# Performance work log

Measured on AMD Instinct MI355X. Metric: run time of the kernel, lower is better.

The kernel has to match this reference:

```python
import jax, jax.numpy as jnp
import numpy as np

MAX_NUM_LEVELS = 3.5
NUM_LEVELS = 4  # mip levels 0..3 (levels clamped to [0, 2.5])


def affine_grid(matrix, N, H, W):
    # F.affine_grid, align_corners=False. matrix: (N,2,3) -> grid (N,H,W,2) in xy order.
    xs = (jnp.arange(W, dtype=jnp.float32) + 0.5) * (2.0 / W) - 1.0
    ys = (jnp.arange(H, dtype=jnp.float32) + 0.5) * (2.0 / H) - 1.0
    gy, gx = jnp.meshgrid(ys, xs, indexing='ij')
    base = jnp.stack([gx, gy, jnp.ones_like(gx)], axis=-1)  # (H,W,3)
    return jnp.einsum('hwk,nik->nhwi', base, matrix)  # (N,H,W,2)


def grid_sample_border(img, grid):
    # bilinear grid_sample, padding_mode='border', align_corners=False
    N, C, H, W = img.shape
    x = (grid[..., 0] + 1.0) * (W / 2.0) - 0.5
    y = (grid[..., 1] + 1.0) * (H / 2.0) - 0.5
    x0 = jnp.floor(x); y0 = jnp.floor(y)
    tx = x - x0; ty = y - y0
    x0i = jnp.clip(x0.astype(jnp.int32), 0, W - 1)
    x1i = jnp.clip(x0.astype(jnp.int32) + 1, 0, W - 1)
    y0i = jnp.clip(y0.astype(jnp.int32), 0, H - 1)
    y1i = jnp.clip(y0.astype(jnp.int32) + 1, 0, H - 1)
    b = jnp.arange(N)[:, None, None]
    g = lambda yi, xi: img[b, :, yi, xi]  # (N,Ho,Wo,C) gather
    out = (g(y0i, x0i) * ((1 - tx) * (1 - ty))[..., None]
           + g(y0i, x1i) * (tx * (1 - ty))[..., None]
           + g(y1i, x0i) * ((1 - tx) * ty)[..., None]
           + g(y1i, x1i) * (tx * ty)[..., None])
    return jnp.transpose(out, (0, 3, 1, 2))  # (N,C,Ho,Wo)


def blur_downsample(x):
    N, C, H, W = x.shape
    k1 = jnp.array([1., 3., 3., 1.], dtype=x.dtype) / 8.0
    k = k1[:, None] * k1[None, :]
    xp = jnp.pad(x, ((0, 0), (0, 0), (1, 2), (1, 2)), mode='reflect')
    kernel = jnp.broadcast_to(k[None, None], (C, 1, 4, 4))
    return jax.lax.conv_general_dilated(xp, kernel, window_strides=(2, 2), padding='VALID',
                                        feature_group_count=C,
                                        dimension_numbers=('NCHW', 'OIHW', 'NCHW'))


def compute_levels(grid, H, W):
    # per-pixel mip LOD from local stretch of the sampling grid (in source pixel units)
    coords = (grid + 1.0) * 0.5 * jnp.array([W, H], dtype=grid.dtype)  # (N,Ho,Wo,2)
    dx = coords[:, :-1, 1:] - coords[:, :-1, :-1]
    dy = coords[:, 1:, :-1] - coords[:, :-1, :-1]
    scale = jnp.maximum(jnp.linalg.norm(dx, axis=-1), jnp.linalg.norm(dy, axis=-1))
    scale = jnp.pad(scale, ((0, 0), (0, 1), (0, 1)), mode='edge')  # (N,Ho,Wo)
    levels = jnp.log2(jnp.maximum(scale, 1.0))
    return jnp.clip(levels, 0.0, MAX_NUM_LEVELS - 1.0)


def mipmap_warp(img, grid):
    N, C, H, W = img.shape
    levels = compute_levels(grid, H, W)  # (N,Ho,Wo)
    pyr = [img]
    for _ in range(NUM_LEVELS - 1):
        pyr.append(blur_downsample(pyr[-1]))
    samples = jnp.stack([grid_sample_border(p, grid) for p in pyr], axis=0)  # (L,N,C,Ho,Wo)
    ls = jnp.arange(NUM_LEVELS, dtype=levels.dtype)[:, None, None, None]
    w = jnp.clip(1.0 - jnp.abs(levels[None] - ls), 0.0, 1.0)  # trilinear blend weights (L,N,Ho,Wo)
    return jnp.einsum('lnhw,lnchw->nchw', w, samples)


def setup_inputs() -> dict:
    key = jax.random.key(0)
    k1, k2, k3 = jax.random.split(key, 3)
    N, C, H, W, D = 64, 3, 256, 256, 512
    img = jax.random.normal(k1, (N, C, H, W), dtype=jnp.float32)
    features = jax.random.normal(k2, (N, D), dtype=jnp.float32)
    # learned head params (zero-init in torch; small random here so the warp is nontrivial)
    lin_w = jax.random.normal(k3, (4, D), dtype=jnp.float32) * 0.02
    lin_b = jnp.zeros((4,), dtype=jnp.float32)
    return {'img': img, 'features': features, 'lin_w': lin_w, 'lin_b': lin_b}


def reference(img, features, lin_w, lin_b):
    params = features @ lin_w.T + lin_b  # (N,4)
    rot = jnp.tanh(params[:, 0:1]) * jnp.pi
    scale = jnp.exp(params[:, 1:2])
    sx, sy = params[:, 2:3], params[:, 3:4]
    c, s = jnp.cos(rot), jnp.sin(rot)
    matrix = jnp.concatenate([scale * c, -scale * s, sx, scale * s, scale * c, sy], axis=1).reshape(-1, 2, 3)
    affine_params = jnp.concatenate([rot, scale, sx, sy], axis=1)
    N, C, H, W = img.shape
    grid = affine_grid(matrix, N, H, W)
    out = mipmap_warp(img, grid)
    return out, grid, matrix, affine_params
```

## Files before the change

### kernel.cpp

```cpp
#include <hip/hip_runtime.h>
#include <math.h>

#define N_B 64
#define C_CH 3
#define H_IMG 256
#define W_IMG 256
#define D_FEAT 512

#define OUT_OFF_GRID   12582912
#define OUT_OFF_MATRIX 20971520
#define OUT_OFF_AFFINE 20971904

#define PYR1_SZ (N_B * 128 * 128 * 3)
#define PYR2_SZ (N_B * 64 * 64 * 3)
#define PYR3_SZ (N_B * 32 * 32 * 3)

typedef float v2f __attribute__((ext_vector_type(2)));
typedef float f4u __attribute__((ext_vector_type(4), aligned(4)));
typedef float f2u __attribute__((ext_vector_type(2), aligned(4)));

__global__ void params_kernel(const float* __restrict__ features,
                              const float* __restrict__ lin_w,
                              const float* __restrict__ lin_b,
                              float* __restrict__ out_matrix,
                              float* __restrict__ out_affine,
                              float* __restrict__ ws_params)
{
    const int n = blockIdx.x;
    const int t = threadIdx.x;
    const float* f = features + n * D_FEAT;
    float f0 = f[t];
    float f1 = f[t + 256];
    float a0 = f0 * lin_w[0 * D_FEAT + t] + f1 * lin_w[0 * D_FEAT + t + 256];
    float a1 = f0 * lin_w[1 * D_FEAT + t] + f1 * lin_w[1 * D_FEAT + t + 256];
    float a2 = f0 * lin_w[2 * D_FEAT + t] + f1 * lin_w[2 * D_FEAT + t + 256];
    float a3 = f0 * lin_w[3 * D_FEAT + t] + f1 * lin_w[3 * D_FEAT + t + 256];

    __shared__ float red[4][256];
    red[0][t] = a0; red[1][t] = a1; red[2][t] = a2; red[3][t] = a3;
    __syncthreads();
    for (int s = 128; s > 0; s >>= 1) {
        if (t < s) {
            red[0][t] += red[0][t + s];
            red[1][t] += red[1][t + s];
            red[2][t] += red[2][t + s];
            red[3][t] += red[3][t + s];
        }
        __syncthreads();
    }
    if (t == 0) {
        float p0 = red[0][0] + lin_b[0];
        float p1 = red[1][0] + lin_b[1];
        float p2 = red[2][0] + lin_b[2];
        float p3 = red[3][0] + lin_b[3];
        float rot   = tanhf(p0) * 3.14159265358979323846f;
        float scale = expf(p1);
        float c = cosf(rot), s = sinf(rot);
        float m00 = scale * c, m01 = -scale * s, m02 = p2;
        float m10 = scale * s, m11 =  scale * c, m12 = p3;
        out_matrix[n * 6 + 0] = m00;
        out_matrix[n * 6 + 1] = m01;
        out_matrix[n * 6 + 2] = m02;
        out_matrix[n * 6 + 3] = m10;
        out_matrix[n * 6 + 4] = m11;
        out_matrix[n * 6 + 5] = m12;
        out_affine[n * 4 + 0] = rot;
        out_affine[n * 4 + 1] = scale;
        out_affine[n * 4 + 2] = p2;
        out_affine[n * 4 + 3] = p3;
        float lv = log2f(fmaxf(scale, 1.0f));
        lv = fminf(fmaxf(lv, 0.0f), 2.5f);
        ws_params[n * 8 + 0] = m00;
        ws_params[n * 8 + 1] = m01;
        ws_params[n * 8 + 2] = m02;
        ws_params[n * 8 + 3] = m10;
        ws_params[n * 8 + 4] = m11;
        ws_params[n * 8 + 5] = m12;
        ws_params[n * 8 + 6] = lv;
        ws_params[n * 8 + 7] = 0.0f;
    }
}

__global__ void down1_kernel(const float* __restrict__ img,
                             float* __restrict__ pyr1,
                             const float* __restrict__ ws_params)
{
    const int n = blockIdx.y;
    if (ws_params[n * 8 + 6] <= 0.0f) return;
    const int p = blockIdx.x * 256 + threadIdx.x;
    const int i = p >> 7;
    const int j = p & 127;

    int r[4];
#pragma unroll
    for (int a = 0; a < 4; a++) {
        int q = 2 * i + a - 1;
        if (q < 0) q = -q;
        if (q >= 256) q = 510 - q;
        r[a] = q;
    }
    const int  cb  = min(max(2 * j - 1, 0), 252);
    const bool jlo = (j == 0);
    const bool jhi = (j == 127);
    const bool je  = jlo || jhi;

    const float* s = img + (size_t)n * 3 * 65536;

    f4u T[3][4];
#pragma unroll
    for (int c = 0; c < 3; c++)
#pragma unroll
        for (int a = 0; a < 4; a++)
            T[c][a] = *(const f4u*)(s + c * 65536 + r[a] * 256 + cb);

    const float k0 = 0.125f, k1 = 0.375f;
    const float kr[4] = {0.125f, 0.375f, 0.375f, 0.125f};
    float o[3];
#pragma unroll
    for (int c = 0; c < 3; c++) {
        float acc = 0.0f;
#pragma unroll
        for (int a = 0; a < 4; a++) {
            f4u A = T[c][a];
            float t0 = je  ? A.y : A.x;
            float t1 = jlo ? A.x : (jhi ? A.z : A.y);
            float t2 = jlo ? A.y : (jhi ? A.w : A.z);
            float t3 = je  ? A.z : A.w;
            float h = k0 * t0 + k1 * t1 + k1 * t2 + k0 * t3;
            acc += kr[a] * h;
        }
        o[c] = acc;
    }
    float* d = pyr1 + (size_t)n * (128 * 128 * 3) + (size_t)p * 3;
    d[0] = o[0]; d[1] = o[1]; d[2] = o[2];
}

template<int Hs, int Ws>
__global__ void downN_kernel(const float* __restrict__ src,
                             float* __restrict__ dst,
                             const float* __restrict__ ws_params,
                             float lvl_gate)
{
    const int n = blockIdx.y;
    if (ws_params[n * 8 + 6] <= lvl_gate) return;
    constexpr int Hd = Hs / 2, Wd = Ws / 2;
    const int p = blockIdx.x * 256 + threadIdx.x;
    const int i = p / Wd;
    const int j = p % Wd;

    int r[4], cc[4];
#pragma unroll
    for (int a = 0; a < 4; a++) {
        int q = 2 * i + a - 1;
        if (q < 0) q = -q;
        if (q >= Hs) q = 2 * Hs - 2 - q;
        r[a] = q;
        int u = 2 * j + a - 1;
        if (u < 0) u = -u;
        if (u >= Ws) u = 2 * Ws - 2 - u;
        cc[a] = u;
    }
    const float* s = src + (size_t)n * 3 * Hs * Ws;
    const int rs = 3 * Ws;

    f4u T[4][4];
#pragma unroll
    for (int a = 0; a < 4; a++)
#pragma unroll
        for (int b = 0; b < 4; b++)
            T[a][b] = *(const f4u*)(s + r[a] * rs + 3 * cc[b]);

    const float k0 = 0.125f, k1 = 0.375f;
    const float kr[4] = {0.125f, 0.375f, 0.375f, 0.125f};
    float o[3];
#pragma unroll
    for (int c = 0; c < 3; c++) {
        float acc = 0.0f;
#pragma unroll
        for (int a = 0; a < 4; a++) {
            float h = k0 * T[a][0][c] + k1 * T[a][1][c]
                    + k1 * T[a][2][c] + k0 * T[a][3][c];
            acc += kr[a] * h;
        }
        o[c] = acc;
    }
    float* d = dst + (size_t)n * 3 * Hd * Wd + (size_t)p * 3;
    d[0] = o[0]; d[1] = o[1]; d[2] = o[2];
}

struct TapSetup {
    const float* row0;
    const float* row1;
    float w00, w01, w10, w11;
    bool selHi0, selLo1;
    size_t planeStride;
};

__device__ __forceinline__ TapSetup make_taps(const float* __restrict__ base, int l,
                                              float X, float Y)
{
    const int Wl = W_IMG >> l;
    const int Hl = H_IMG >> l;
    float x = (X + 1.0f) * (0.5f * (float)Wl) - 0.5f;
    float y = (Y + 1.0f) * (0.5f * (float)Hl) - 0.5f;
    float x0f = floorf(x), y0f = floorf(y);
    float tx = x - x0f, ty = y - y0f;
    int x0 = (int)x0f, y0 = (int)y0f;
    int y0i = min(max(y0,     0), Hl - 1);
    int y1i = min(max(y0 + 1, 0), Hl - 1);
    int xp = min(max(x0, 0), Wl - 2);
    TapSetup ts;
    ts.row0 = base + (size_t)y0i * Wl + xp;
    ts.row1 = base + (size_t)y1i * Wl + xp;
    ts.selHi0 = (x0 >= Wl - 1);
    ts.selLo1 = (x0 < 0);
    ts.w00 = (1.0f - tx) * (1.0f - ty);
    ts.w01 = tx * (1.0f - ty);
    ts.w10 = (1.0f - tx) * ty;
    ts.w11 = tx * ty;
    ts.planeStride = (size_t)Hl * Wl;
    return ts;
}

__device__ __forceinline__ float tap_eval(const TapSetup& ts, float2 a, float2 b)
{
    float t00 = ts.selHi0 ? a.y : a.x;
    float t01 = ts.selLo1 ? a.x : a.y;
    float t10 = ts.selHi0 ? b.y : b.x;
    float t11 = ts.selLo1 ? b.x : b.y;
    return ts.w00 * t00 + ts.w01 * t01 + ts.w10 * t10 + ts.w11 * t11;
}

struct NTap {
    const float* r0;
    const float* r1;
    float w00, w01, w10, w11;
    bool hi, lo;
};

__device__ __forceinline__ NTap make_ntap(const float* __restrict__ base, int l,
                                          float X, float Y)
{
    const int Wl = W_IMG >> l;
    const int Hl = H_IMG >> l;
    float x = (X + 1.0f) * (0.5f * (float)Wl) - 0.5f;
    float y = (Y + 1.0f) * (0.5f * (float)Hl) - 0.5f;
    float x0f = floorf(x), y0f = floorf(y);
    float tx = x - x0f, ty = y - y0f;
    int x0 = (int)x0f, y0 = (int)y0f;
    int y0i = min(max(y0,     0), Hl - 1);
    int y1i = min(max(y0 + 1, 0), Hl - 1);
    int xp  = min(max(x0, 0), Wl - 2);
    const int rs = 3 * Wl;
    NTap t;
    t.r0 = base + (size_t)y0i * rs + 3 * xp;
    t.r1 = base + (size_t)y1i * rs + 3 * xp;
    t.hi = (x0 >= Wl - 1);
    t.lo = (x0 < 0);
    t.w00 = (1.0f - tx) * (1.0f - ty);
    t.w01 = tx * (1.0f - ty);
    t.w10 = (1.0f - tx) * ty;
    t.w11 = tx * ty;
    return t;
}

__device__ __forceinline__ void ntap_eval(const NTap& t, f4u a, f2u a2,
                                          f4u b, f2u b2, float* v)
{
    float e0[6] = {a.x, a.y, a.z, a.w, a2.x, a2.y};
    float e1[6] = {b.x, b.y, b.z, b.w, b2.x, b2.y};
#pragma unroll
    for (int c = 0; c < 3; c++) {
        float p00 = t.hi ? e0[c + 3] : e0[c];
        float p01 = t.lo ? e0[c]     : e0[c + 3];
        float p10 = t.hi ? e1[c + 3] : e1[c];
        float p11 = t.lo ? e1[c]     : e1[c + 3];
        v[c] = t.w00 * p00 + t.w01 * p01 + t.w10 * p10 + t.w11 * p11;
    }
}

__device__ __forceinline__ const float* npyr(int l, const float* p1,
                                             const float* p2, const float* p3,
                                             int n)
{
    if (l == 1) return p1 + (size_t)n * (128 * 128 * 3);
    if (l == 2) return p2 + (size_t)n * (64 * 64 * 3);
    return p3 + (size_t)n * (32 * 32 * 3);
}

__global__ __launch_bounds__(256, 4)
void warp_kernel(const float* __restrict__ img,
                 const float* __restrict__ pyr1,
                 const float* __restrict__ pyr2,
                 const float* __restrict__ pyr3,
                 const float* __restrict__ ws_params,
                 float* __restrict__ out,
                 float* __restrict__ gridOut)
{
    const int n = blockIdx.y;
    const int tile = blockIdx.x;
    const int tid = threadIdx.x;
    const int w0 = (tile & 7) << 5;
    const int h0 = (tile >> 3) << 3;
    const int w = w0 + (((tid >> 6) & 1) << 4) + (tid & 15);
    const int h = h0 + ((tid >> 7) << 2) + ((tid >> 4) & 3);

    const float* P = ws_params + n * 8;
    float m00 = P[0], m01 = P[1], m02 = P[2];
    float m10 = P[3], m11 = P[4], m12 = P[5];
    float lv  = P[6];

    float gx = ((float)w + 0.5f) * (2.0f / (float)W_IMG) - 1.0f;
    float gy = ((float)h + 0.5f) * (2.0f / (float)H_IMG) - 1.0f;
    float X = m00 * gx + m01 * gy + m02;
    float Y = m10 * gx + m11 * gy + m12;

    v2f gp = {X, Y};
    __builtin_nontemporal_store(gp, (v2f*)gridOut + ((size_t)(n * H_IMG + h) * W_IMG + w));

    int   l0   = (int)lv;
    float frac = lv - (float)l0;
    const bool hasL1 = (frac > 0.0f);
    const float wA = 1.0f - frac;

    size_t obase = ((size_t)n * C_CH * H_IMG + h) * W_IMG + w;

    if (l0 == 0) {
        const float* base0 = img + (size_t)n * 3 * 65536;
        TapSetup t0 = make_taps(base0, 0, X, Y);
        float2 A0[3], B0[3];
#pragma unroll
        for (int c = 0; c < 3; c++) {
            A0[c] = *(const float2*)(t0.row0 + c * t0.planeStride);
            B0[c] = *(const float2*)(t0.row1 + c * t0.planeStride);
        }
        if (hasL1) {
            NTap t1 = make_ntap(pyr1 + (size_t)n * (128 * 128 * 3), 1, X, Y);
            f4u a = *(const f4u*)t1.r0;  f2u a2 = *(const f2u*)(t1.r0 + 4);
            f4u b = *(const f4u*)t1.r1;  f2u b2 = *(const f2u*)(t1.r1 + 4);
            float v1[3];
            ntap_eval(t1, a, a2, b, b2, v1);
#pragma unroll
            for (int c = 0; c < 3; c++) {
                float v0 = tap_eval(t0, A0[c], B0[c]);
                __builtin_nontemporal_store(wA * v0 + frac * v1[c],
                                            out + obase + (size_t)c * 65536);
            }
        } else {
#pragma unroll
            for (int c = 0; c < 3; c++)
                __builtin_nontemporal_store(tap_eval(t0, A0[c], B0[c]),
                                            out + obase + (size_t)c * 65536);
        }
    } else {
        const float* base0 = npyr(l0, pyr1, pyr2, pyr3, n);
        NTap t0 = make_ntap(base0, l0, X, Y);
        f4u a = *(const f4u*)t0.r0;  f2u a2 = *(const f2u*)(t0.r0 + 4);
        f4u b = *(const f4u*)t0.r1;  f2u b2 = *(const f2u*)(t0.r1 + 4);
        if (hasL1) {
            const float* base1 = npyr(l0 + 1, pyr1, pyr2, pyr3, n);
            NTap t1 = make_ntap(base1, l0 + 1, X, Y);
            f4u c1 = *(const f4u*)t1.r0;  f2u c2 = *(const f2u*)(t1.r0 + 4);
            f4u d1 = *(const f4u*)t1.r1;  f2u d2 = *(const f2u*)(t1.r1 + 4);
            float v0[3], v1[3];
            ntap_eval(t0, a, a2, b, b2, v0);
            ntap_eval(t1, c1, c2, d1, d2, v1);
#pragma unroll
            for (int c = 0; c < 3; c++)
                __builtin_nontemporal_store(wA * v0[c] + frac * v1[c],
                                            out + obase + (size_t)c * 65536);
        } else {
            float v0[3];
            ntap_eval(t0, a, a2, b, b2, v0);
#pragma unroll
            for (int c = 0; c < 3; c++)
                __builtin_nontemporal_store(v0[c],
                                            out + obase + (size_t)c * 65536);
        }
    }
}

extern "C" void kernel_launch(void* const* d_in, const int* in_sizes, int n_in,
                              void* d_out, int out_size, void* d_ws, size_t ws_size,
                              hipStream_t stream)
{
    const float* img      = (const float*)d_in[0];
    const float* features = (const float*)d_in[1];
    const float* lin_w    = (const float*)d_in[2];
    const float* lin_b    = (const float*)d_in[3];

    float* out        = (float*)d_out;
    float* gridOut    = out + OUT_OFF_GRID;
    float* out_matrix = out + OUT_OFF_MATRIX;
    float* out_affine = out + OUT_OFF_AFFINE;

    float* ws        = (float*)d_ws;
    float* ws_params = ws;
    float* pyr1 = ws + 1024;
    float* pyr2 = pyr1 + PYR1_SZ;
    float* pyr3 = pyr2 + PYR2_SZ;

    params_kernel<<<N_B, 256, 0, stream>>>(features, lin_w, lin_b,
                                           out_matrix, out_affine, ws_params);

    down1_kernel<<<dim3(64, N_B), 256, 0, stream>>>(img, pyr1, ws_params);
    downN_kernel<128, 128><<<dim3(16, N_B), 256, 0, stream>>>(pyr1, pyr2, ws_params, 1.0f);
    downN_kernel<64, 64><<<dim3(4, N_B), 256, 0, stream>>>(pyr2, pyr3, ws_params, 2.0f);

    warp_kernel<<<dim3(H_IMG * W_IMG / 256, N_B), 256, 0, stream>>>(
        img, pyr1, pyr2, pyr3, ws_params, out, gridOut);
}
```

Baseline: 166.7 us.

## Compute four outputs per thread in down1 and two rows per thread in warp

The first downsample kernel now has each thread produce four adjacent level-1 pixels from two vector loads plus two edge scalars per row. This shares horizontal taps across outputs and writes results with three 16-byte stores instead of scattered scalar stores. The warp kernel processes two output rows per thread (rows h and h+8), halving the grid and issuing both sets of loads before evaluating them to raise memory-level parallelism. The cost is higher register pressure under the existing launch bounds and fewer blocks per kernel.

```diff
diff --git a/kernel.cpp b/kernel.cpp
--- a/kernel.cpp
+++ b/kernel.cpp
@@ -87,9 +87,9 @@
 {
     const int n = blockIdx.y;
     if (ws_params[n * 8 + 6] <= 0.0f) return;
-    const int p = blockIdx.x * 256 + threadIdx.x;
-    const int i = p >> 7;
-    const int j = p & 127;
+    const int idx = blockIdx.x * 256 + threadIdx.x;
+    const int t = idx & 31;
+    const int i = idx >> 5;
 
     int r[4];
 #pragma unroll
@@ -99,40 +99,48 @@
         if (q >= 256) q = 510 - q;
         r[a] = q;
     }
-    const int  cb  = min(max(2 * j - 1, 0), 252);
-    const bool jlo = (j == 0);
-    const bool jhi = (j == 127);
-    const bool je  = jlo || jhi;
+    const int c8 = 8 * t;
+    const int li = (t > 0)  ? c8 - 1 : 1;
+    const int ri = (t < 31) ? c8 + 8 : 254;
 
     const float* s = img + (size_t)n * 3 * 65536;
-
-    f4u T[3][4];
-#pragma unroll
-    for (int c = 0; c < 3; c++)
-#pragma unroll
-        for (int a = 0; a < 4; a++)
-            T[c][a] = *(const f4u*)(s + c * 65536 + r[a] * 256 + cb);
 
     const float k0 = 0.125f, k1 = 0.375f;
     const float kr[4] = {0.125f, 0.375f, 0.375f, 0.125f};
-    float o[3];
-#pragma unroll
-    for (int c = 0; c < 3; c++) {
-        float acc = 0.0f;
-#pragma unroll
-        for (int a = 0; a < 4; a++) {
-            f4u A = T[c][a];
-            float t0 = je  ? A.y : A.x;
-            float t1 = jlo ? A.x : (jhi ? A.z : A.y);
-            float t2 = jlo ? A.y : (jhi ? A.w : A.z);
-            float t3 = je  ? A.z : A.w;
-            float h = k0 * t0 + k1 * t1 + k1 * t2 + k0 * t3;
-            acc += kr[a] * h;
-        }
-        o[c] = acc;
-    }
-    float* d = pyr1 + (size_t)n * (128 * 128 * 3) + (size_t)p * 3;
-    d[0] = o[0]; d[1] = o[1]; d[2] = o[2];
+
+    float acc[3][4] = {};
+#pragma unroll
+    for (int a = 0; a < 4; a++) {
+        const float* rbase = s + (size_t)r[a] * 256;
+        f4u A[3], B[3];
+        float L[3], R[3];
+#pragma unroll
+        for (int c = 0; c < 3; c++) {
+            const float* row = rbase + c * 65536;
+            A[c] = *(const f4u*)(row + c8);
+            B[c] = *(const f4u*)(row + c8 + 4);
+            L[c] = row[li];
+            R[c] = row[ri];
+        }
+#pragma unroll
+        for (int c = 0; c < 3; c++) {
+            float h0 = k0 * L[c]   + k1 * A[c].x + k1 * A[c].y + k0 * A[c].z;
+            float h1 = k0 * A[c].y + k1 * A[c].z + k1 * A[c].w + k0 * B[c].x;
+            float h2 = k0 * A[c].w + k1 * B[c].x + k1 * B[c].y + k0 * B[c].z;
+            float h3 = k0 * B[c].y + k1 * B[c].z + k1 * B[c].w + k0 * R[c];
+            acc[c][0] += kr[a] * h0;
+            acc[c][1] += kr[a] * h1;
+            acc[c][2] += kr[a] * h2;
+            acc[c][3] += kr[a] * h3;
+        }
+    }
+    float* d = pyr1 + (size_t)n * (128 * 128 * 3) + ((size_t)i * 128 + 4 * t) * 3;
+    f4u s0 = {acc[0][0], acc[1][0], acc[2][0], acc[0][1]};
+    f4u s1 = {acc[1][1], acc[2][1], acc[0][2], acc[1][2]};
+    f4u s2 = {acc[2][2], acc[0][3], acc[1][3], acc[2][3]};
+    *(f4u*)(d)     = s0;
+    *(f4u*)(d + 4) = s1;
+    *(f4u*)(d + 8) = s2;
 }
 
 template<int Hs, int Ws>
@@ -264,11 +272,20 @@
     return t;
 }
 
-__device__ __forceinline__ void ntap_eval(const NTap& t, f4u a, f2u a2,
-                                          f4u b, f2u b2, float* v)
-{
-    float e0[6] = {a.x, a.y, a.z, a.w, a2.x, a2.y};
-    float e1[6] = {b.x, b.y, b.z, b.w, b2.x, b2.y};
+struct NPay { f4u a; f2u a2; f4u b; f2u b2; };
+
+__device__ __forceinline__ NPay ntap_load(const NTap& t)
+{
+    NPay p;
+    p.a  = *(const f4u*)t.r0;  p.a2 = *(const f2u*)(t.r0 + 4);
+    p.b  = *(const f4u*)t.r1;  p.b2 = *(const f2u*)(t.r1 + 4);
+    return p;
+}
+
+__device__ __forceinline__ void ntap_eval(const NTap& t, const NPay& p, float* v)
+{
+    float e0[6] = {p.a.x, p.a.y, p.a.z, p.a.w, p.a2.x, p.a2.y};
+    float e1[6] = {p.b.x, p.b.y, p.b.z, p.b.w, p.b2.x, p.b2.y};
 #pragma unroll
     for (int c = 0; c < 3; c++) {
         float p00 = t.hi ? e0[c + 3] : e0[c];
@@ -301,81 +318,111 @@
     const int tile = blockIdx.x;
     const int tid = threadIdx.x;
     const int w0 = (tile & 7) << 5;
-    const int h0 = (tile >> 3) << 3;
-    const int w = w0 + (((tid >> 6) & 1) << 4) + (tid & 15);
-    const int h = h0 + ((tid >> 7) << 2) + ((tid >> 4) & 3);
+    const int h0 = (tile >> 3) << 4;
+    const int w  = w0 + (((tid >> 6) & 1) << 4) + (tid & 15);
+    const int ha = h0 + ((tid >> 7) << 2) + ((tid >> 4) & 3);
+    const int hb = ha + 8;
 
     const float* P = ws_params + n * 8;
     float m00 = P[0], m01 = P[1], m02 = P[2];
     float m10 = P[3], m11 = P[4], m12 = P[5];
     float lv  = P[6];
 
-    float gx = ((float)w + 0.5f) * (2.0f / (float)W_IMG) - 1.0f;
-    float gy = ((float)h + 0.5f) * (2.0f / (float)H_IMG) - 1.0f;
-    float X = m00 * gx + m01 * gy + m02;
-    float Y = m10 * gx + m11 * gy + m12;
-
-    v2f gp = {X, Y};
-    __builtin_nontemporal_store(gp, (v2f*)gridOut + ((size_t)(n * H_IMG + h) * W_IMG + w));
+    float gx  = ((float)w + 0.5f) * (2.0f / (float)W_IMG) - 1.0f;
+    float gya = ((float)ha + 0.5f) * (2.0f / (float)H_IMG) - 1.0f;
+    float gyb = ((float)hb + 0.5f) * (2.0f / (float)H_IMG) - 1.0f;
+    float Xa = m00 * gx + m01 * gya + m02;
+    float Ya = m10 * gx + m11 * gya + m12;
+    float Xb = m00 * gx + m01 * gyb + m02;
+    float Yb = m10 * gx + m11 * gyb + m12;
+
+    v2f gpa = {Xa, Ya}, gpb = {Xb, Yb};
+    __builtin_nontemporal_store(gpa, (v2f*)gridOut + ((size_t)(n * H_IMG + ha) * W_IMG + w));
+    __builtin_nontemporal_store(gpb, (v2f*)gridOut + ((size_t)(n * H_IMG + hb) * W_IMG + w));
 
     int   l0   = (int)lv;
     float frac = lv - (float)l0;
     const bool hasL1 = (frac > 0.0f);
     const float wA = 1.0f - frac;
 
-    size_t obase = ((size_t)n * C_CH * H_IMG + h) * W_IMG + w;
+    size_t oba = ((size_t)n * C_CH * H_IMG + ha) * W_IMG + w;
+    size_t obb = ((size_t)n * C_CH * H_IMG + hb) * W_IMG + w;
 
     if (l0 == 0) {
         const float* base0 = img + (size_t)n * 3 * 65536;
-        TapSetup t0 = make_taps(base0, 0, X, Y);
-        float2 A0[3], B0[3];
+        TapSetup ta = make_taps(base0, 0, Xa, Ya);
+        TapSetup tb = make_taps(base0, 0, Xb, Yb);
+        float2 Aa[3], Ba[3], Ab[3], Bb[3];
 #pragma unroll
         for (int c = 0; c < 3; c++) {
-            A0[c] = *(const float2*)(t0.row0 + c * t0.planeStride);
-            B0[c] = *(const float2*)(t0.row1 + c * t0.planeStride);
+            Aa[c] = *(const float2*)(ta.row0 + c * 65536);
+            Ba[c] = *(const float2*)(ta.row1 + c * 65536);
+        }
+#pragma unroll
+        for (int c = 0; c < 3; c++) {
+            Ab[c] = *(const float2*)(tb.row0 + c * 65536);
+            Bb[c] = *(const float2*)(tb.row1 + c * 65536);
         }
         if (hasL1) {
-            NTap t1 = make_ntap(pyr1 + (size_t)n * (128 * 128 * 3), 1, X, Y);
-            f4u a = *(const f4u*)t1.r0;  f2u a2 = *(const f2u*)(t1.r0 + 4);
-            f4u b = *(const f4u*)t1.r1;  f2u b2 = *(const f2u*)(t1.r1 + 4);
-            float v1[3];
-            ntap_eval(t1, a, a2, b, b2, v1);
+            const float* b1 = pyr1 + (size_t)n * (128 * 128 * 3);
+            NTap ua = make_ntap(b1, 1, Xa, Ya);
+            NTap ub = make_ntap(b1, 1, Xb, Yb);
+            NPay pa = ntap_load(ua);
+            NPay pb = ntap_load(ub);
+            float v1a[3], v1b[3];
+            ntap_eval(ua, pa, v1a);
+            ntap_eval(ub, pb, v1b);
 #pragma unroll
             for (int c = 0; c < 3; c++) {
-                float v0 = tap_eval(t0, A0[c], B0[c]);
-                __builtin_nontemporal_store(wA * v0 + frac * v1[c],
-                                            out + obase + (size_t)c * 65536);
+                float v0a = tap_eval(ta, Aa[c], Ba[c]);
+                float v0b = tap_eval(tb, Ab[c], Bb[c]);
+                __builtin_nontemporal_store(wA * v0a + frac * v1a[c],
+                                            out + oba + (size_t)c * 65536);
+                __builtin_nontemporal_store(wA * v0b + frac * v1b[c],
+                                            out + obb + (size_t)c * 65536);
             }
         } else {
 #pragma unroll
-            for (int c = 0; c < 3; c++)
-                __builtin_nontemporal_store(tap_eval(t0, A0[c], B0[c]),
-                                            out + obase + (size_t)c * 65536);
+            for (int c = 0; c < 3; c++) {
+                __builtin_nontemporal_store(tap_eval(ta, Aa[c], Ba[c]),
+                                            out + oba + (size_t)c * 65536);
+                __builtin_nontemporal_store(tap_eval(tb, Ab[c], Bb[c]),
+                                            out + obb + (size_t)c * 65536);
+            }
         }
     } else {
         const float* base0 = npyr(l0, pyr1, pyr2, pyr3, n);
-        NTap t0 = make_ntap(base0, l0, X, Y);
-        f4u a = *(const f4u*)t0.r0;  f2u a2 = *(const f2u*)(t0.r0 + 4);
-        f4u b = *(const f4u*)t0.r1;  f2u b2 = *(const f2u*)(t0.r1 + 4);
+        NTap ta = make_ntap(base0, l0, Xa, Ya);
+        NTap tb = make_ntap(base0, l0, Xb, Yb);
+        NPay pa = ntap_load(ta);
+        NPay pb = ntap_load(tb);
         if (hasL1) {
             const float* base1 = npyr(l0 + 1, pyr1, pyr2, pyr3, n);
-            NTap t1 = make_ntap(base1, l0 + 1, X, Y);
-            f4u c1 = *(const f4u*)t1.r0;  f2u c2 = *(const f2u*)(t1.r0 + 4);
-            f4u d1 = *(const f4u*)t1.r1;  f2u d2 = *(const f2u*)(t1.r1 + 4);
-            float v0[3], v1[3];
-            ntap_eval(t0, a, a2, b, b2, v0);
-            ntap_eval(t1, c1, c2, d1, d2, v1);
-#pragma unroll
-            for (int c = 0; c < 3; c++)
-                __builtin_nontemporal_store(wA * v0[c] + frac * v1[c],
-                                            out + obase + (size_t)c * 65536);
+            NTap ua = make_ntap(base1, l0 + 1, Xa, Ya);
+            NTap ub = make_ntap(base1, l0 + 1, Xb, Yb);
+            NPay qa = ntap_load(ua);
+            NPay qb = ntap_load(ub);
+            float v0a[3], v0b[3], v1a[3], v1b[3];
+            ntap_eval(ta, pa, v0a);
+            ntap_eval(tb, pb, v0b);
+            ntap_eval(ua, qa, v1a);
+            ntap_eval(ub, qb, v1b);
+#pragma unroll
+            for (int c = 0; c < 3; c++) {
+                __builtin_nontemporal_store(wA * v0a[c] + frac * v1a[c],
+                                            out + oba + (size_t)c * 65536);
+                __builtin_nontemporal_store(wA * v0b[c] + frac * v1b[c],
+                                            out + obb + (size_t)c * 65536);
+            }
         } else {
-            float v0[3];
-            ntap_eval(t0, a, a2, b, b2, v0);
-#pragma unroll
-            for (int c = 0; c < 3; c++)
-                __builtin_nontemporal_store(v0[c],
-                                            out + obase + (size_t)c * 65536);
+            float v0a[3], v0b[3];
+            ntap_eval(ta, pa, v0a);
+            ntap_eval(tb, pb, v0b);
+#pragma unroll
+            for (int c = 0; c < 3; c++) {
+                __builtin_nontemporal_store(v0a[c], out + oba + (size_t)c * 65536);
+                __builtin_nontemporal_store(v0b[c], out + obb + (size_t)c * 65536);
+            }
         }
     }
 }
@@ -403,10 +450,10 @@
     params_kernel<<<N_B, 256, 0, stream>>>(features, lin_w, lin_b,
                                            out_matrix, out_affine, ws_params);
 
-    down1_kernel<<<dim3(64, N_B), 256, 0, stream>>>(img, pyr1, ws_params);
+    down1_kernel<<<dim3(16, N_B), 256, 0, stream>>>(img, pyr1, ws_params);
     downN_kernel<128, 128><<<dim3(16, N_B), 256, 0, stream>>>(pyr1, pyr2, ws_params, 1.0f);
     downN_kernel<64, 64><<<dim3(4, N_B), 256, 0, stream>>>(pyr2, pyr3, ws_params, 2.0f);
 
-    warp_kernel<<<dim3(H_IMG * W_IMG / 256, N_B), 256, 0, stream>>>(
+    warp_kernel<<<dim3(H_IMG * W_IMG / 512, N_B), 256, 0, stream>>>(
         img, pyr1, pyr2, pyr3, ws_params, out, gridOut);
 }
```

Result: slower. 173.6 us (+4.2%).
